# Kernel tuning notes

Measured on AMD Instinct MI355X. Metric: run time of the kernel, lower is better.

## Reference

```python
import jax, jax.numpy as jnp
import numpy as np

D_BINS = 88
DEPTH_MIN, DEPTH_MAX = 1.0, 45.0
BN_EPS = 1e-5


def setup_inputs() -> dict:
    key = jax.random.key(0)
    ks = jax.random.split(key, 8)
    N, C, H, W = 12, 256, 32, 88
    CC = 128  # context channels
    return {
        "x": jax.random.normal(ks[0], (N, C, H, W), dtype=jnp.float32),
        "dnet_w": jax.random.normal(ks[1], (D_BINS + CC, C), dtype=jnp.float32) * 0.05,
        "dnet_b": jax.random.normal(ks[2], (D_BINS + CC,), dtype=jnp.float32) * 0.05,
        "proj_w": jax.random.normal(ks[3], (C, CC), dtype=jnp.float32) * 0.05,
        "bn_gamma": jax.random.uniform(ks[4], (C,), dtype=jnp.float32) + 0.5,
        "bn_beta": jax.random.normal(ks[5], (C,), dtype=jnp.float32) * 0.1,
        "bn_mean": jax.random.normal(ks[6], (C,), dtype=jnp.float32) * 0.1,
        "bn_var": jax.random.uniform(ks[7], (C,), dtype=jnp.float32) + 0.5,
    }


def reference(x, dnet_w, dnet_b, proj_w, bn_gamma, bn_beta, bn_mean, bn_var):
    # depth_net: 1x1 conv == per-pixel matmul over channels
    dc = jnp.einsum('nchw,oc->nohw', x, dnet_w) + dnet_b[None, :, None, None]
    depth_logits = dc[:, :D_BINS]          # [N, D, H, W]
    tran_feat = dc[:, D_BINS:]             # [N, CC, H, W]
    # context_proj (1x1 conv, no bias) + BatchNorm2d (inference) + exact GELU
    tran_feat = jnp.einsum('nkhw,ck->nchw', tran_feat, proj_w)
    inv_std = jax.lax.rsqrt(bn_var + BN_EPS)
    tran_feat = (tran_feat - bn_mean[None, :, None, None]) * (bn_gamma * inv_std)[None, :, None, None] \
                + bn_beta[None, :, None, None]
    tran_feat = jax.nn.gelu(tran_feat, approximate=False)
    depth_prob = jax.nn.softmax(depth_logits, axis=1)  # [N, D, H, W]
    depth_values = jnp.linspace(DEPTH_MIN, DEPTH_MAX, D_BINS)
    depth_weight = depth_values / depth_values.mean()  # [D]
    # collapse_z=True: bev[n,c,h,w] = tran_feat[n,c,h,w] * sum_d depth_prob[n,d,h,w]*w[d]
    # (fused form of the [N,C,D,H,W] outer-product volume followed by sum over D)
    s = jnp.einsum('ndhw,d->nhw', depth_prob, depth_weight)  # [N, H, W]
    bev = tran_feat * s[:, None, :, :]
    return bev, depth_logits, depth_prob
```

## Files before the change

### kernel.cpp

```cpp
#include <hip/hip_runtime.h>
#include <hip/hip_bf16.h>
#include <math.h>

#define C_IN 256
#define CC 128
#define NDEPTH 88
#define HW 2816
#define NB 12
#define TILE 32
#define NTILES 88
#define LOG_OFF   ((size_t)8650752)
#define PROB_OFF  ((size_t)11624448)

typedef __attribute__((ext_vector_type(8))) short bf16x8;
typedef __attribute__((ext_vector_type(4))) float f32x4;

__device__ __forceinline__ unsigned short f2bf(float f) {
    unsigned int u = __float_as_uint(f);
    unsigned int r = (u + 0x7fffu + ((u >> 16) & 1u)) >> 16;
    return (unsigned short)r;
}
__device__ __forceinline__ unsigned int pack2(float a, float b) {
    return (unsigned int)f2bf(a) | ((unsigned int)f2bf(b) << 16);
}
__device__ __forceinline__ void bar_lgkm() {
    asm volatile("s_waitcnt lgkmcnt(0)\n\ts_barrier" ::: "memory");
}
__device__ __forceinline__ float gelu_fast(float v) {
    float u = v * (1.5957691216f + 0.07135481283f * v * v);
    return v / (1.f + __expf(-u));
}

__global__ void prep_kernel(const float* __restrict__ dnet_w,
                            const float* __restrict__ proj_w,
                            const float* __restrict__ gamma,
                            const float* __restrict__ beta,
                            const float* __restrict__ mean,
                            const float* __restrict__ var,
                            unsigned short* __restrict__ w1d,
                            unsigned short* __restrict__ w1t,
                            unsigned short* __restrict__ projb,
                            float* __restrict__ scale,
                            float* __restrict__ shift) {
    const int tid = blockIdx.x * blockDim.x + threadIdx.x;
    const int total = 96 * 256 + 128 * 256 + 256 * 128;
    for (int idx = tid; idx < total; idx += gridDim.x * blockDim.x) {
        if (idx < 96 * 256) {
            int o = idx >> 8, c = idx & 255;
            w1d[idx] = (o < NDEPTH) ? f2bf(dnet_w[o * 256 + c]) : (unsigned short)0;
        } else if (idx < 96 * 256 + 128 * 256) {
            int j = idx - 96 * 256;
            w1t[j] = f2bf(dnet_w[(NDEPTH + (j >> 8)) * 256 + (j & 255)]);
        } else {
            int j = idx - 96 * 256 - 128 * 256;
            projb[j] = f2bf(proj_w[j]);
        }
    }
    if (tid < 256) {
        float sc = gamma[tid] * rsqrtf(var[tid] + 1e-5f);
        scale[tid] = sc;
        shift[tid] = beta[tid] - mean[tid] * sc;
    }
}

__global__ __launch_bounds__(512, 6)
void fused_kernel(const float* __restrict__ x,
                  const float* __restrict__ dnet_b,
                  const unsigned short* __restrict__ w1d,
                  const unsigned short* __restrict__ w1t,
                  const unsigned short* __restrict__ projb,
                  const float* __restrict__ scale,
                  const float* __restrict__ shift,
                  float* __restrict__ out) {
    __shared__ __align__(16) char buf[28672];
    __shared__ __align__(16) unsigned short trs[2][16 * 128];
    __shared__ float ss[2][16];
    __shared__ float biasd[96];
    __shared__ float biast[128];
    __shared__ float sc_s[256];
    __shared__ float sh_s[256];

    unsigned short* xs = (unsigned short*)buf;
    f32x4* part = (f32x4*)buf;

    const int bid = blockIdx.x;
    const int n   = bid / NTILES;
    const int hw0 = (bid % NTILES) * TILE;
    const int t    = threadIdx.x;
    const int lane = t & 63;
    const int wv   = t >> 6;
    const int khalf = wv >> 2;
    const int sub   = wv & 3;
    const int strip = sub >> 1;
    const int role  = sub & 1;

    if (t < 96)       biasd[t] = (t < NDEPTH) ? dnet_b[t] : 0.f;
    else if (t < 224) biast[t - 96] = dnet_b[t - 8];
    if (t < 256) { sc_s[t] = scale[t]; sh_s[t] = shift[t]; }

    {
        const int hwl = t & 31;
        const int cg  = t >> 5;
        const float* xb = x + (size_t)n * C_IN * HW + hw0 + hwl;
        #pragma unroll
        for (int cb = 0; cb < 2; ++cb) {
            const int c0 = cb * 128 + cg * 8;
            float f[8];
            #pragma unroll
            for (int j = 0; j < 8; ++j) f[j] = xb[(size_t)(c0 + j) * HW];
            uint4 v;
            v.x = pack2(f[0], f[1]);
            v.y = pack2(f[2], f[3]);
            v.z = pack2(f[4], f[5]);
            v.w = pack2(f[6], f[7]);
            const int csw = (c0 >> 3) ^ (hwl & 7);
            *reinterpret_cast<uint4*>(&xs[hwl * 256 + csw * 8]) = v;
        }
    }
    bar_lgkm();

    const int g = lane >> 4;
    const int m = lane & 15;
    const int brow  = strip * 16 + m;
    const int hwcol = hw0 + strip * 16 + m;

    if (role == 0) {
        f32x4 accd[6];
        #pragma unroll
        for (int i = 0; i < 6; ++i) accd[i] = (f32x4){0.f, 0.f, 0.f, 0.f};
        #pragma unroll
        for (int ksl = 0; ksl < 4; ++ksl) {
            const int k0 = (khalf * 4 + ksl) * 32;
            const int csw = ((k0 >> 3) + g) ^ (brow & 7);
            bf16x8 b = *reinterpret_cast<const bf16x8*>(&xs[brow * 256 + csw * 8]);
            #pragma unroll
            for (int dt = 0; dt < 6; ++dt) {
                bf16x8 a = *reinterpret_cast<const bf16x8*>(&w1d[(dt * 16 + m) * 256 + k0 + g * 8]);
                accd[dt] = __builtin_amdgcn_mfma_f32_16x16x32_bf16(a, b, accd[dt], 0, 0, 0);
            }
        }
        bar_lgkm();
        if (khalf == 1) {
            #pragma unroll
            for (int dt = 0; dt < 6; ++dt)
                part[(strip * 14 + dt) * 64 + lane] = accd[dt];
        }
        bar_lgkm();
        if (khalf == 0) {
            #pragma unroll
            for (int dt = 0; dt < 6; ++dt)
                accd[dt] += part[(strip * 14 + dt) * 64 + lane];
            #pragma unroll
            for (int dt = 0; dt < 6; ++dt) {
                #pragma unroll
                for (int r = 0; r < 4; ++r)
                    accd[dt][r] += biasd[dt * 16 + g * 4 + r];
            }
            float mx = -1e30f;
            #pragma unroll
            for (int dt = 0; dt < 6; ++dt) {
                #pragma unroll
                for (int r = 0; r < 4; ++r) {
                    const int o = dt * 16 + g * 4 + r;
                    if (o < NDEPTH) mx = fmaxf(mx, accd[dt][r]);
                }
            }
            mx = fmaxf(mx, __shfl_xor(mx, 16));
            mx = fmaxf(mx, __shfl_xor(mx, 32));
            float sum = 0.f, spn = 0.f;
            #pragma unroll
            for (int dt = 0; dt < 6; ++dt) {
                #pragma unroll
                for (int r = 0; r < 4; ++r) {
                    const int o = dt * 16 + g * 4 + r;
                    if (o < NDEPTH) {
                        float e = __expf(accd[dt][r] - mx);
                        sum += e;
                        spn += e * ((1.f + (float)o * (44.f / 87.f)) * (1.f / 23.f));
                    }
                }
            }
            sum += __shfl_xor(sum, 16);
            sum += __shfl_xor(sum, 32);
            spn += __shfl_xor(spn, 16);
            spn += __shfl_xor(spn, 32);
            const float inv = 1.0f / sum;
            if (lane < 16) ss[strip][m] = spn * inv;
            float* lg = out + LOG_OFF  + (size_t)n * NDEPTH * HW + hwcol;
            float* pb = out + PROB_OFF + (size_t)n * NDEPTH * HW + hwcol;
            #pragma unroll
            for (int dt = 0; dt < 6; ++dt) {
                #pragma unroll
                for (int r = 0; r < 4; ++r) {
                    const int o = dt * 16 + g * 4 + r;
                    if (o < NDEPTH) {
                        lg[(size_t)o * HW] = accd[dt][r];
                        pb[(size_t)o * HW] = __expf(accd[dt][r] - mx) * inv;
                    }
                }
            }
        }
    } else {
        f32x4 acct[8];
        #pragma unroll
        for (int i = 0; i < 8; ++i) acct[i] = (f32x4){0.f, 0.f, 0.f, 0.f};
        #pragma unroll
        for (int ksl = 0; ksl < 4; ++ksl) {
            const int k0 = (khalf * 4 + ksl) * 32;
            const int csw = ((k0 >> 3) + g) ^ (brow & 7);
            bf16x8 b = *reinterpret_cast<const bf16x8*>(&xs[brow * 256 + csw * 8]);
            #pragma unroll
            for (int tt = 0; tt < 8; ++tt) {
                bf16x8 a = *reinterpret_cast<const bf16x8*>(&w1t[(tt * 16 + m) * 256 + k0 + g * 8]);
                acct[tt] = __builtin_amdgcn_mfma_f32_16x16x32_bf16(a, b, acct[tt], 0, 0, 0);
            }
        }
        bar_lgkm();
        if (khalf == 1) {
            #pragma unroll
            for (int tt = 0; tt < 8; ++tt)
                part[(strip * 14 + 6 + tt) * 64 + lane] = acct[tt];
        }
        bar_lgkm();
        if (khalf == 0) {
            #pragma unroll
            for (int tt = 0; tt < 8; ++tt)
                acct[tt] += part[(strip * 14 + 6 + tt) * 64 + lane];
            unsigned short* tw = &trs[strip][0];
            #pragma unroll
            for (int tt = 0; tt < 8; ++tt) {
                const int cb = tt * 16 + g * 4;
                float v0 = acct[tt][0] + biast[cb + 0];
                float v1 = acct[tt][1] + biast[cb + 1];
                float v2 = acct[tt][2] + biast[cb + 2];
                float v3 = acct[tt][3] + biast[cb + 3];
                const int csw = (cb >> 3) ^ (m & 7);
                uint2 pkd;
                pkd.x = pack2(v0, v1);
                pkd.y = pack2(v2, v3);
                *reinterpret_cast<uint2*>(&tw[m * 128 + csw * 8 + (g & 1) * 4]) = pkd;
            }
        }
    }
    bar_lgkm();

    const int strip2 = wv >> 2;
    const int ctb    = (wv & 3) * 4;
    const int hwcol2 = hw0 + strip2 * 16 + m;
    f32x4 acc2[4];
    #pragma unroll
    for (int i = 0; i < 4; ++i) acc2[i] = (f32x4){0.f, 0.f, 0.f, 0.f};
    {
        const unsigned short* tw = &trs[strip2][0];
        #pragma unroll
        for (int ks = 0; ks < 4; ++ks) {
            const int k0 = ks * 32;
            const int csw = ((k0 >> 3) + g) ^ (m & 7);
            bf16x8 b = *reinterpret_cast<const bf16x8*>(&tw[m * 128 + csw * 8]);
            #pragma unroll
            for (int ct = 0; ct < 4; ++ct) {
                bf16x8 a = *reinterpret_cast<const bf16x8*>(&projb[((ctb + ct) * 16 + m) * 128 + k0 + g * 8]);
                acc2[ct] = __builtin_amdgcn_mfma_f32_16x16x32_bf16(a, b, acc2[ct], 0, 0, 0);
            }
        }
    }

    {
        const float sp = ss[strip2][m];
        float* bev = out + (size_t)n * C_IN * HW + hwcol2;
        #pragma unroll
        for (int ct = 0; ct < 4; ++ct) {
            #pragma unroll
            for (int r = 0; r < 4; ++r) {
                const int cc = (ctb + ct) * 16 + g * 4 + r;
                float v  = acc2[ct][r] * sc_s[cc] + sh_s[cc];
                bev[(size_t)cc * HW] = gelu_fast(v) * sp;
            }
        }
    }
}

extern "C" void kernel_launch(void* const* d_in, const int* in_sizes, int n_in,
                              void* d_out, int out_size, void* d_ws, size_t ws_size,
                              hipStream_t stream) {
    const float* x      = (const float*)d_in[0];
    const float* dnet_w = (const float*)d_in[1];
    const float* dnet_b = (const float*)d_in[2];
    const float* proj_w = (const float*)d_in[3];
    const float* gamma  = (const float*)d_in[4];
    const float* beta   = (const float*)d_in[5];
    const float* mean   = (const float*)d_in[6];
    const float* var    = (const float*)d_in[7];
    float* out = (float*)d_out;

    char* ws = (char*)d_ws;
    unsigned short* w1d   = (unsigned short*)ws;
    unsigned short* w1t   = (unsigned short*)(ws + 49152);
    unsigned short* projb = (unsigned short*)(ws + 49152 + 65536);
    float* scale = (float*)(ws + 49152 + 65536 + 65536);
    float* shift = scale + 256;

    prep_kernel<<<96, 256, 0, stream>>>(dnet_w, proj_w, gamma, beta, mean, var,
                                        w1d, w1t, projb, scale, shift);
    fused_kernel<<<NB * NTILES, 512, 0, stream>>>(x, dnet_b, w1d, w1t, projb,
                                                  scale, shift, out);
}
```

Before: 155.4 us.

## Double pixel tile, pre-swizzle weights into MFMA fragment order, rebalance wave roles

The pixel tile per block goes from 32 to 64, halving the grid. Each wave now computes both depth and context outputs for one 16-pixel strip over half of K, instead of waves being split by role. The prep kernel stores weights already in per-lane MFMA fragment order, so each lane loads them with one contiguous 16-byte read. Logit and probability stores move after the BEV stores. LDS per block doubles and launch bounds drop to 4 blocks, which cuts occupancy and leaves fewer blocks for load balancing.

```diff
diff --git a/kernel.cpp b/kernel.cpp
--- a/kernel.cpp
+++ b/kernel.cpp
@@ -7,8 +7,8 @@
 #define NDEPTH 88
 #define HW 2816
 #define NB 12
-#define TILE 32
-#define NTILES 88
+#define TILE 64
+#define NTILES 44
 #define LOG_OFF   ((size_t)8650752)
 #define PROB_OFF  ((size_t)11624448)
 
@@ -37,23 +37,44 @@
                             const float* __restrict__ beta,
                             const float* __restrict__ mean,
                             const float* __restrict__ var,
-                            unsigned short* __restrict__ w1d,
-                            unsigned short* __restrict__ w1t,
-                            unsigned short* __restrict__ projb,
+                            uint4* __restrict__ w1df,
+                            uint4* __restrict__ w1tf,
+                            uint4* __restrict__ projf,
                             float* __restrict__ scale,
                             float* __restrict__ shift) {
     const int tid = blockIdx.x * blockDim.x + threadIdx.x;
-    const int total = 96 * 256 + 128 * 256 + 256 * 128;
-    for (int idx = tid; idx < total; idx += gridDim.x * blockDim.x) {
-        if (idx < 96 * 256) {
-            int o = idx >> 8, c = idx & 255;
-            w1d[idx] = (o < NDEPTH) ? f2bf(dnet_w[o * 256 + c]) : (unsigned short)0;
-        } else if (idx < 96 * 256 + 128 * 256) {
-            int j = idx - 96 * 256;
-            w1t[j] = f2bf(dnet_w[(NDEPTH + (j >> 8)) * 256 + (j & 255)]);
+    const int N1 = 48 * 64, N2 = 64 * 64, N3 = 64 * 64;
+    for (int e = tid; e < N1 + N2 + N3; e += gridDim.x * blockDim.x) {
+        uint4 v = {0u, 0u, 0u, 0u};
+        if (e < N1) {
+            const int fb = e >> 6, l = e & 63;
+            const int kh = fb / 24, rem = fb % 24, ks = rem / 6, dt = rem % 6;
+            const int m = l & 15, g = l >> 4;
+            const int o = dt * 16 + m;
+            if (o < NDEPTH) {
+                const float* p = dnet_w + o * 256 + kh * 128 + ks * 32 + g * 8;
+                v.x = pack2(p[0], p[1]); v.y = pack2(p[2], p[3]);
+                v.z = pack2(p[4], p[5]); v.w = pack2(p[6], p[7]);
+            }
+            w1df[e] = v;
+        } else if (e < N1 + N2) {
+            const int e2 = e - N1;
+            const int fb = e2 >> 6, l = e2 & 63;
+            const int kh = fb / 32, rem = fb % 32, ks = rem / 8, tt = rem % 8;
+            const int m = l & 15, g = l >> 4;
+            const float* p = dnet_w + (NDEPTH + tt * 16 + m) * 256 + kh * 128 + ks * 32 + g * 8;
+            v.x = pack2(p[0], p[1]); v.y = pack2(p[2], p[3]);
+            v.z = pack2(p[4], p[5]); v.w = pack2(p[6], p[7]);
+            w1tf[e2] = v;
         } else {
-            int j = idx - 96 * 256 - 128 * 256;
-            projb[j] = f2bf(proj_w[j]);
+            const int e3 = e - N1 - N2;
+            const int fb = e3 >> 6, l = e3 & 63;
+            const int ks = fb >> 4, ct = fb & 15;
+            const int m = l & 15, g = l >> 4;
+            const float* p = proj_w + (ct * 16 + m) * 128 + ks * 32 + g * 8;
+            v.x = pack2(p[0], p[1]); v.y = pack2(p[2], p[3]);
+            v.z = pack2(p[4], p[5]); v.w = pack2(p[6], p[7]);
+            projf[e3] = v;
         }
     }
     if (tid < 256) {
@@ -63,48 +84,47 @@
     }
 }
 
-__global__ __launch_bounds__(512, 6)
+__global__ __launch_bounds__(512, 4)
 void fused_kernel(const float* __restrict__ x,
                   const float* __restrict__ dnet_b,
-                  const unsigned short* __restrict__ w1d,
-                  const unsigned short* __restrict__ w1t,
-                  const unsigned short* __restrict__ projb,
+                  const uint4* __restrict__ w1df,
+                  const uint4* __restrict__ w1tf,
+                  const uint4* __restrict__ projf,
                   const float* __restrict__ scale,
                   const float* __restrict__ shift,
                   float* __restrict__ out) {
-    __shared__ __align__(16) char buf[28672];
-    __shared__ __align__(16) unsigned short trs[2][16 * 128];
-    __shared__ float ss[2][16];
+    __shared__ __align__(16) char buf[57344];
+    __shared__ __align__(16) unsigned short trs[4][16 * 128];
+    __shared__ float ss[4][16];
     __shared__ float biasd[96];
     __shared__ float biast[128];
     __shared__ float sc_s[256];
     __shared__ float sh_s[256];
 
     unsigned short* xs = (unsigned short*)buf;
-    f32x4* part = (f32x4*)buf;
+    f32x4* partD = (f32x4*)buf;
+    f32x4* partT = (f32x4*)(buf + 24576);
 
     const int bid = blockIdx.x;
     const int n   = bid / NTILES;
     const int hw0 = (bid % NTILES) * TILE;
-    const int t    = threadIdx.x;
-    const int lane = t & 63;
-    const int wv   = t >> 6;
+    const int t     = threadIdx.x;
+    const int lane  = t & 63;
+    const int wv    = t >> 6;
+    const int strip = wv & 3;
     const int khalf = wv >> 2;
-    const int sub   = wv & 3;
-    const int strip = sub >> 1;
-    const int role  = sub & 1;
 
     if (t < 96)       biasd[t] = (t < NDEPTH) ? dnet_b[t] : 0.f;
     else if (t < 224) biast[t - 96] = dnet_b[t - 8];
     if (t < 256) { sc_s[t] = scale[t]; sh_s[t] = shift[t]; }
 
     {
-        const int hwl = t & 31;
-        const int cg  = t >> 5;
+        const int hwl = t & 63;
+        const int cg  = t >> 6;
         const float* xb = x + (size_t)n * C_IN * HW + hw0 + hwl;
         #pragma unroll
-        for (int cb = 0; cb < 2; ++cb) {
-            const int c0 = cb * 128 + cg * 8;
+        for (int cb = 0; cb < 4; ++cb) {
+            const int c0 = cb * 64 + cg * 8;
             float f[8];
             #pragma unroll
             for (int j = 0; j < 8; ++j) f[j] = xb[(size_t)(c0 + j) * HW];
@@ -124,10 +144,14 @@
     const int brow  = strip * 16 + m;
     const int hwcol = hw0 + strip * 16 + m;
 
-    if (role == 0) {
-        f32x4 accd[6];
-        #pragma unroll
-        for (int i = 0; i < 6; ++i) accd[i] = (f32x4){0.f, 0.f, 0.f, 0.f};
+    f32x4 accd[6], acct[8];
+    #pragma unroll
+    for (int i = 0; i < 6; ++i) accd[i] = (f32x4){0.f, 0.f, 0.f, 0.f};
+    #pragma unroll
+    for (int i = 0; i < 8; ++i) acct[i] = (f32x4){0.f, 0.f, 0.f, 0.f};
+    {
+        const bf16x8* w1dv = (const bf16x8*)w1df;
+        const bf16x8* w1tv = (const bf16x8*)w1tf;
         #pragma unroll
         for (int ksl = 0; ksl < 4; ++ksl) {
             const int k0 = (khalf * 4 + ksl) * 32;
@@ -135,146 +159,135 @@
             bf16x8 b = *reinterpret_cast<const bf16x8*>(&xs[brow * 256 + csw * 8]);
             #pragma unroll
             for (int dt = 0; dt < 6; ++dt) {
-                bf16x8 a = *reinterpret_cast<const bf16x8*>(&w1d[(dt * 16 + m) * 256 + k0 + g * 8]);
+                bf16x8 a = w1dv[((khalf * 4 + ksl) * 6 + dt) * 64 + lane];
                 accd[dt] = __builtin_amdgcn_mfma_f32_16x16x32_bf16(a, b, accd[dt], 0, 0, 0);
             }
-        }
-        bar_lgkm();
-        if (khalf == 1) {
-            #pragma unroll
-            for (int dt = 0; dt < 6; ++dt)
-                part[(strip * 14 + dt) * 64 + lane] = accd[dt];
-        }
-        bar_lgkm();
-        if (khalf == 0) {
-            #pragma unroll
-            for (int dt = 0; dt < 6; ++dt)
-                accd[dt] += part[(strip * 14 + dt) * 64 + lane];
-            #pragma unroll
-            for (int dt = 0; dt < 6; ++dt) {
-                #pragma unroll
-                for (int r = 0; r < 4; ++r)
-                    accd[dt][r] += biasd[dt * 16 + g * 4 + r];
-            }
-            float mx = -1e30f;
-            #pragma unroll
-            for (int dt = 0; dt < 6; ++dt) {
-                #pragma unroll
-                for (int r = 0; r < 4; ++r) {
-                    const int o = dt * 16 + g * 4 + r;
-                    if (o < NDEPTH) mx = fmaxf(mx, accd[dt][r]);
+            #pragma unroll
+            for (int tt = 0; tt < 8; ++tt) {
+                bf16x8 a = w1tv[((khalf * 4 + ksl) * 8 + tt) * 64 + lane];
+                acct[tt] = __builtin_amdgcn_mfma_f32_16x16x32_bf16(a, b, acct[tt], 0, 0, 0);
+            }
+        }
+    }
+    bar_lgkm();
+
+    if (khalf == 0) {
+        #pragma unroll
+        for (int tt = 0; tt < 8; ++tt)
+            partT[(strip * 8 + tt) * 64 + lane] = acct[tt];
+    } else {
+        #pragma unroll
+        for (int dt = 0; dt < 6; ++dt)
+            partD[(strip * 6 + dt) * 64 + lane] = accd[dt];
+    }
+    bar_lgkm();
+
+    float mx = 0.f, inv = 0.f;
+    if (khalf == 0) {
+        #pragma unroll
+        for (int dt = 0; dt < 6; ++dt) {
+            accd[dt] += partD[(strip * 6 + dt) * 64 + lane];
+            #pragma unroll
+            for (int r = 0; r < 4; ++r)
+                accd[dt][r] += biasd[dt * 16 + g * 4 + r];
+        }
+        mx = -1e30f;
+        #pragma unroll
+        for (int dt = 0; dt < 6; ++dt) {
+            #pragma unroll
+            for (int r = 0; r < 4; ++r) {
+                const int o = dt * 16 + g * 4 + r;
+                if (o < NDEPTH) mx = fmaxf(mx, accd[dt][r]);
+            }
+        }
+        mx = fmaxf(mx, __shfl_xor(mx, 16));
+        mx = fmaxf(mx, __shfl_xor(mx, 32));
+        float sum = 0.f, spn = 0.f;
+        #pragma unroll
+        for (int dt = 0; dt < 6; ++dt) {
+            #pragma unroll
+            for (int r = 0; r < 4; ++r) {
+                const int o = dt * 16 + g * 4 + r;
+                if (o < NDEPTH) {
+                    float e = __expf(accd[dt][r] - mx);
+                    sum += e;
+                    spn += e * ((1.f + (float)o * (44.f / 87.f)) * (1.f / 23.f));
                 }
             }
-            mx = fmaxf(mx, __shfl_xor(mx, 16));
-            mx = fmaxf(mx, __shfl_xor(mx, 32));
-            float sum = 0.f, spn = 0.f;
-            #pragma unroll
-            for (int dt = 0; dt < 6; ++dt) {
-                #pragma unroll
-                for (int r = 0; r < 4; ++r) {
-                    const int o = dt * 16 + g * 4 + r;
-                    if (o < NDEPTH) {
-                        float e = __expf(accd[dt][r] - mx);
-                        sum += e;
-                        spn += e * ((1.f + (float)o * (44.f / 87.f)) * (1.f / 23.f));
-                    }
-                }
-            }
-            sum += __shfl_xor(sum, 16);
-            sum += __shfl_xor(sum, 32);
-            spn += __shfl_xor(spn, 16);
-            spn += __shfl_xor(spn, 32);
-            const float inv = 1.0f / sum;
-            if (lane < 16) ss[strip][m] = spn * inv;
-            float* lg = out + LOG_OFF  + (size_t)n * NDEPTH * HW + hwcol;
-            float* pb = out + PROB_OFF + (size_t)n * NDEPTH * HW + hwcol;
-            #pragma unroll
-            for (int dt = 0; dt < 6; ++dt) {
-                #pragma unroll
-                for (int r = 0; r < 4; ++r) {
-                    const int o = dt * 16 + g * 4 + r;
-                    if (o < NDEPTH) {
-                        lg[(size_t)o * HW] = accd[dt][r];
-                        pb[(size_t)o * HW] = __expf(accd[dt][r] - mx) * inv;
-                    }
-                }
-            }
-        }
+        }
+        sum += __shfl_xor(sum, 16);
+        sum += __shfl_xor(sum, 32);
+        spn += __shfl_xor(spn, 16);
+        spn += __shfl_xor(spn, 32);
+        inv = 1.0f / sum;
+        if (lane < 16) ss[strip][m] = spn * inv;
     } else {
-        f32x4 acct[8];
-        #pragma unroll
-        for (int i = 0; i < 8; ++i) acct[i] = (f32x4){0.f, 0.f, 0.f, 0.f};
-        #pragma unroll
-        for (int ksl = 0; ksl < 4; ++ksl) {
-            const int k0 = (khalf * 4 + ksl) * 32;
-            const int csw = ((k0 >> 3) + g) ^ (brow & 7);
-            bf16x8 b = *reinterpret_cast<const bf16x8*>(&xs[brow * 256 + csw * 8]);
-            #pragma unroll
-            for (int tt = 0; tt < 8; ++tt) {
-                bf16x8 a = *reinterpret_cast<const bf16x8*>(&w1t[(tt * 16 + m) * 256 + k0 + g * 8]);
-                acct[tt] = __builtin_amdgcn_mfma_f32_16x16x32_bf16(a, b, acct[tt], 0, 0, 0);
-            }
-        }
-        bar_lgkm();
-        if (khalf == 1) {
-            #pragma unroll
-            for (int tt = 0; tt < 8; ++tt)
-                part[(strip * 14 + 6 + tt) * 64 + lane] = acct[tt];
-        }
-        bar_lgkm();
-        if (khalf == 0) {
-            #pragma unroll
-            for (int tt = 0; tt < 8; ++tt)
-                acct[tt] += part[(strip * 14 + 6 + tt) * 64 + lane];
-            unsigned short* tw = &trs[strip][0];
-            #pragma unroll
-            for (int tt = 0; tt < 8; ++tt) {
-                const int cb = tt * 16 + g * 4;
-                float v0 = acct[tt][0] + biast[cb + 0];
-                float v1 = acct[tt][1] + biast[cb + 1];
-                float v2 = acct[tt][2] + biast[cb + 2];
-                float v3 = acct[tt][3] + biast[cb + 3];
-                const int csw = (cb >> 3) ^ (m & 7);
-                uint2 pkd;
-                pkd.x = pack2(v0, v1);
-                pkd.y = pack2(v2, v3);
-                *reinterpret_cast<uint2*>(&tw[m * 128 + csw * 8 + (g & 1) * 4]) = pkd;
-            }
+        #pragma unroll
+        for (int tt = 0; tt < 8; ++tt)
+            acct[tt] += partT[(strip * 8 + tt) * 64 + lane];
+        unsigned short* tw = &trs[strip][0];
+        #pragma unroll
+        for (int tt = 0; tt < 8; ++tt) {
+            const int cb = tt * 16 + g * 4;
+            float v0 = acct[tt][0] + biast[cb + 0];
+            float v1 = acct[tt][1] + biast[cb + 1];
+            float v2 = acct[tt][2] + biast[cb + 2];
+            float v3 = acct[tt][3] + biast[cb + 3];
+            const int csw = (cb >> 3) ^ (m & 7);
+            uint2 pkd;
+            pkd.x = pack2(v0, v1);
+            pkd.y = pack2(v2, v3);
+            *reinterpret_cast<uint2*>(&tw[m * 128 + csw * 8 + (g & 1) * 4]) = pkd;
         }
     }
     bar_lgkm();
 
-    const int strip2 = wv >> 2;
-    const int ctb    = (wv & 3) * 4;
-    const int hwcol2 = hw0 + strip2 * 16 + m;
-    f32x4 acc2[4];
+    const int ctb = khalf * 8;
+    f32x4 acc2[8];
     #pragma unroll
-    for (int i = 0; i < 4; ++i) acc2[i] = (f32x4){0.f, 0.f, 0.f, 0.f};
+    for (int i = 0; i < 8; ++i) acc2[i] = (f32x4){0.f, 0.f, 0.f, 0.f};
     {
-        const unsigned short* tw = &trs[strip2][0];
+        const bf16x8* pv = (const bf16x8*)projf;
+        const unsigned short* tw = &trs[strip][0];
         #pragma unroll
         for (int ks = 0; ks < 4; ++ks) {
             const int k0 = ks * 32;
             const int csw = ((k0 >> 3) + g) ^ (m & 7);
             bf16x8 b = *reinterpret_cast<const bf16x8*>(&tw[m * 128 + csw * 8]);
             #pragma unroll
-            for (int ct = 0; ct < 4; ++ct) {
-                bf16x8 a = *reinterpret_cast<const bf16x8*>(&projb[((ctb + ct) * 16 + m) * 128 + k0 + g * 8]);
+            for (int ct = 0; ct < 8; ++ct) {
+                bf16x8 a = pv[(ks * 16 + ctb + ct) * 64 + lane];
                 acc2[ct] = __builtin_amdgcn_mfma_f32_16x16x32_bf16(a, b, acc2[ct], 0, 0, 0);
             }
         }
     }
 
     {
-        const float sp = ss[strip2][m];
-        float* bev = out + (size_t)n * C_IN * HW + hwcol2;
-        #pragma unroll
-        for (int ct = 0; ct < 4; ++ct) {
+        const float sp = ss[strip][m];
+        float* bev = out + (size_t)n * C_IN * HW + hwcol;
+        #pragma unroll
+        for (int ct = 0; ct < 8; ++ct) {
             #pragma unroll
             for (int r = 0; r < 4; ++r) {
                 const int cc = (ctb + ct) * 16 + g * 4 + r;
                 float v  = acc2[ct][r] * sc_s[cc] + sh_s[cc];
                 bev[(size_t)cc * HW] = gelu_fast(v) * sp;
+            }
+        }
+    }
+
+    if (khalf == 0) {
+        float* lg = out + LOG_OFF  + (size_t)n * NDEPTH * HW + hwcol;
+        float* pb = out + PROB_OFF + (size_t)n * NDEPTH * HW + hwcol;
+        #pragma unroll
+        for (int dt = 0; dt < 6; ++dt) {
+            #pragma unroll
+            for (int r = 0; r < 4; ++r) {
+                const int o = dt * 16 + g * 4 + r;
+                if (o < NDEPTH) {
+                    lg[(size_t)o * HW] = accd[dt][r];
+                    pb[(size_t)o * HW] = __expf(accd[dt][r] - mx) * inv;
+                }
             }
         }
     }
@@ -294,14 +307,14 @@
     float* out = (float*)d_out;
 
     char* ws = (char*)d_ws;
-    unsigned short* w1d   = (unsigned short*)ws;
-    unsigned short* w1t   = (unsigned short*)(ws + 49152);
-    unsigned short* projb = (unsigned short*)(ws + 49152 + 65536);
+    uint4* w1df = (uint4*)ws;
+    uint4* w1tf = (uint4*)(ws + 49152);
+    uint4* projf = (uint4*)(ws + 49152 + 65536);
     float* scale = (float*)(ws + 49152 + 65536 + 65536);
     float* shift = scale + 256;
 
     prep_kernel<<<96, 256, 0, stream>>>(dnet_w, proj_w, gamma, beta, mean, var,
-                                        w1d, w1t, projb, scale, shift);
-    fused_kernel<<<NB * NTILES, 512, 0, stream>>>(x, dnet_b, w1d, w1t, projb,
+                                        w1df, w1tf, projf, scale, shift);
+    fused_kernel<<<NB * NTILES, 512, 0, stream>>>(x, dnet_b, w1df, w1tf, projf,
                                                   scale, shift, out);
 }
```

Result: faster. 129.0 us (-17.0%).
